# Kernel optimization log

Hardware: AMD Instinct MI355X
Metric: run time of the kernel (lower is better)

## Reference

```python
import jax, jax.numpy as jnp
import numpy as np

N_NODES = 120000  # n_entities + n_users
N_REL = 16
D = 64   # entity_dim
R = 64   # relation_dim
E = 1600000


def setup_inputs() -> dict:
    key = jax.random.key(0)
    k1, k2, k3, k4, k5, k6 = jax.random.split(key, 6)
    return {
        "entity_user_embed": jax.random.normal(k1, (N_NODES, D), dtype=jnp.float32) * 0.1,
        "relation_embed": jax.random.normal(k2, (N_REL, R), dtype=jnp.float32) * 0.1,
        "W_R": jax.random.normal(k3, (N_REL, D, R), dtype=jnp.float32) * 0.1,
        "edge_src": jax.random.randint(k4, (E,), 0, N_NODES, dtype=jnp.int32),
        "edge_dst": jax.random.randint(k5, (E,), 0, N_NODES, dtype=jnp.int32),
        "edge_type": jax.random.randint(k6, (E,), 0, N_REL, dtype=jnp.int32),
    }


def reference(entity_user_embed, relation_embed, W_R, edge_src, edge_dst, edge_type):
    n_nodes = entity_user_embed.shape[0]
    # Per-relation transform of every node embedding: [n_rel, n_nodes, R].
    # Equivalent to the per-relation edge loop: matmul(emb[id], W_R[r]).
    trans = jnp.einsum('nd,rdk->rnk', entity_user_embed, W_R)
    r_mul_t = trans[edge_type, edge_src]   # [E, R] (edges.src path)
    r_mul_h = trans[edge_type, edge_dst]   # [E, R] (edges.dst path)
    r_embed = relation_embed[edge_type]    # [E, R]
    # bmm([E,1,R], [E,R,1]) -> per-edge dot product
    att = jnp.sum(r_mul_t * jnp.tanh(r_mul_h + r_embed), axis=-1)  # [E]
    # edge softmax over incoming edges of each destination node
    att_max = jax.ops.segment_max(att, edge_dst, num_segments=n_nodes)
    ex = jnp.exp(att - att_max[edge_dst])
    denom = jax.ops.segment_sum(ex, edge_dst, num_segments=n_nodes)
    out = ex / denom[edge_dst]
    return out[:, None]  # [E, 1], matching squeeze(-1) of [E,1,1]
```

## Files before the change

kernel.cpp:

```cpp
#include <hip/hip_runtime.h>
#include <hip/hip_bf16.h>

#define D64 64
#define NREL 16
#define SCALE 32.0f
#define INV_SCALE 0.03125f

typedef __attribute__((ext_vector_type(8))) short bf16x8;
typedef __attribute__((ext_vector_type(4))) float f32x4;
typedef __attribute__((ext_vector_type(2))) float f32x2;

__device__ __forceinline__ float tanh_fast(float x) {
    float e = __expf(2.0f * x);
    return 1.0f - 2.0f / (e + 1.0f);
}

__device__ __forceinline__ float tanh_poly(float x) {
    x = fmaxf(-1.5f, fminf(1.5f, x));
    float u = x * x;
    float p = fmaf(u, -0.0182227f, 0.108952f);
    p = fmaf(u, p, -0.329139f);
    p = fmaf(u, p, 1.0f);
    return x * p;
}

__device__ __forceinline__ unsigned short f2b(float x) {
    __hip_bfloat16 h = __float2bfloat16(x);
    return *reinterpret_cast<unsigned short*>(&h);
}

__global__ void prep_kernel(const float* __restrict__ WR, const float* __restrict__ rel,
                            unsigned short* __restrict__ Wt, float* __restrict__ relp,
                            float* __restrict__ denom, int n_nodes) {
    int i = blockIdx.x * blockDim.x + threadIdx.x;
    if (i < NREL * D64 * D64) {
        int r = i >> 12, mt = (i >> 10) & 3, q2 = (i >> 9) & 1;
        int ln = (i >> 3) & 63, j = i & 7;
        int c = mt * 16 + (ln & 15);
        int d = q2 * 32 + ((ln >> 4) << 3) + j;
        Wt[i] = f2b(WR[(r << 12) + (d << 6) + c] * SCALE);
    }
    if (i < NREL * D64) {
        int t = i >> 6, kp = i & 63;
        int q = kp >> 4, m = (kp >> 2) & 3, g = kp & 3;
        relp[i] = rel[t * D64 + m * 16 + q * 4 + g];
    }
    if (i < n_nodes) denom[i] = 0.0f;
}

__global__ __launch_bounds__(256, 3)
void trans_gemm_kernel(const float* __restrict__ emb,
                       const unsigned short* __restrict__ Wt,
                       uint4* __restrict__ trans,
                       int n_nodes) {
    const int tid  = threadIdx.x;
    const int lane = tid & 63;
    const int wid  = tid >> 6;
    const int col  = lane & 15;
    const int quad = lane >> 4;
    const int rbase = (blockIdx.x & 1) * 8;
    const int nodebase = (blockIdx.x >> 1) * 256 + wid * 64;

    bf16x8 bfr[4][2];
    int nds[4];
    #pragma unroll
    for (int j = 0; j < 4; ++j) {
        int node = nodebase + j * 16 + col;
        nds[j] = node;
        int cn = node < n_nodes ? node : n_nodes - 1;
        const float* bp = emb + (size_t)cn * D64 + quad * 8;
        #pragma unroll
        for (int ks = 0; ks < 2; ++ks) {
            float4 v0 = *(const float4*)(bp + ks * 32);
            float4 v1 = *(const float4*)(bp + ks * 32 + 4);
            bfr[j][ks][0] = (short)f2b(v0.x); bfr[j][ks][1] = (short)f2b(v0.y);
            bfr[j][ks][2] = (short)f2b(v0.z); bfr[j][ks][3] = (short)f2b(v0.w);
            bfr[j][ks][4] = (short)f2b(v1.x); bfr[j][ks][5] = (short)f2b(v1.y);
            bfr[j][ks][6] = (short)f2b(v1.z); bfr[j][ks][7] = (short)f2b(v1.w);
        }
    }

    const unsigned short* wb = Wt + (rbase << 12) + (lane << 3);

    #pragma unroll 1
    for (int rr = 0; rr < 8; ++rr) {
        const int r = rbase + rr;
        const unsigned short* lb = wb + (rr << 12);
        f32x4 acc[4][4];
        #pragma unroll
        for (int mt = 0; mt < 4; ++mt) {
            bf16x8 a0 = *(const bf16x8*)(lb + (mt << 10));
            bf16x8 a1 = *(const bf16x8*)(lb + (mt << 10) + 512);
            #pragma unroll
            for (int j = 0; j < 4; ++j) {
                f32x4 c = {0.f, 0.f, 0.f, 0.f};
                c = __builtin_amdgcn_mfma_f32_16x16x32_bf16(a0, bfr[j][0], c, 0, 0, 0);
                c = __builtin_amdgcn_mfma_f32_16x16x32_bf16(a1, bfr[j][1], c, 0, 0, 0);
                acc[mt][j] = c;
            }
        }
        #pragma unroll
        for (int j = 0; j < 4; ++j) {
            if (nds[j] < n_nodes) {
                uint4 pk;
                unsigned p;
                p = __builtin_amdgcn_cvt_pk_fp8_f32(acc[0][j][0], acc[0][j][1], 0, false);
                p = __builtin_amdgcn_cvt_pk_fp8_f32(acc[0][j][2], acc[0][j][3], p, true);
                pk.x = p;
                p = __builtin_amdgcn_cvt_pk_fp8_f32(acc[1][j][0], acc[1][j][1], 0, false);
                p = __builtin_amdgcn_cvt_pk_fp8_f32(acc[1][j][2], acc[1][j][3], p, true);
                pk.y = p;
                p = __builtin_amdgcn_cvt_pk_fp8_f32(acc[2][j][0], acc[2][j][1], 0, false);
                p = __builtin_amdgcn_cvt_pk_fp8_f32(acc[2][j][2], acc[2][j][3], p, true);
                pk.z = p;
                p = __builtin_amdgcn_cvt_pk_fp8_f32(acc[3][j][0], acc[3][j][1], 0, false);
                p = __builtin_amdgcn_cvt_pk_fp8_f32(acc[3][j][2], acc[3][j][3], p, true);
                pk.w = p;
                trans[((size_t)r * n_nodes + nds[j]) * 4 + quad] = pk;
            }
        }
    }
}

__device__ __forceinline__ void term4(unsigned ut, unsigned uh, float4 r, float& acc) {
    f32x2 tlo = __builtin_amdgcn_cvt_pk_f32_fp8(ut, false);
    f32x2 thi = __builtin_amdgcn_cvt_pk_f32_fp8(ut, true);
    f32x2 hlo = __builtin_amdgcn_cvt_pk_f32_fp8(uh, false);
    f32x2 hhi = __builtin_amdgcn_cvt_pk_f32_fp8(uh, true);
    acc += tlo[0] * tanh_poly(fmaf(hlo[0], INV_SCALE, r.x));
    acc += tlo[1] * tanh_poly(fmaf(hlo[1], INV_SCALE, r.y));
    acc += thi[0] * tanh_poly(fmaf(hhi[0], INV_SCALE, r.z));
    acc += thi[1] * tanh_poly(fmaf(hhi[1], INV_SCALE, r.w));
}

__global__ __launch_bounds__(256)
void edge_kernel(const unsigned* __restrict__ trans,
                 const float* __restrict__ relp,
                 const int* __restrict__ esrc, const int* __restrict__ edst,
                 const int* __restrict__ etype,
                 float* __restrict__ out, float* __restrict__ denom,
                 int E, int n_nodes) {
    int e0 = blockIdx.x * 512 + threadIdx.x;
    int e1 = e0 + 256;
    bool v0 = e0 < E, v1 = e1 < E;
    int i0 = v0 ? e0 : 0;
    int i1 = v1 ? e1 : 0;
    int t0 = etype[i0], s0 = esrc[i0], d0 = edst[i0];
    int t1 = etype[i1], s1 = esrc[i1], d1 = edst[i1];

    const uint4* tb = (const uint4*)trans;
    unsigned nn = (unsigned)n_nodes;
    unsigned rt0 = ((unsigned)t0 * nn + (unsigned)s0) * 4u;
    unsigned rh0 = ((unsigned)t0 * nn + (unsigned)d0) * 4u;
    unsigned rt1 = ((unsigned)t1 * nn + (unsigned)s1) * 4u;
    unsigned rh1 = ((unsigned)t1 * nn + (unsigned)d1) * 4u;

    uint4 T0[4], H0[4], T1[4], H1[4];
    #pragma unroll
    for (int c4 = 0; c4 < 4; ++c4) {
        T0[c4] = tb[rt0 + c4]; H0[c4] = tb[rh0 + c4];
        T1[c4] = tb[rt1 + c4]; H1[c4] = tb[rh1 + c4];
    }

    const float4* pr0 = (const float4*)(relp + t0 * D64);
    const float4* pr1 = (const float4*)(relp + t1 * D64);
    float a0 = 0.f, a1 = 0.f;
    #pragma unroll
    for (int c4 = 0; c4 < 4; ++c4) {
        term4(T0[c4].x, H0[c4].x, pr0[c4 * 4 + 0], a0);
        term4(T1[c4].x, H1[c4].x, pr1[c4 * 4 + 0], a1);
        term4(T0[c4].y, H0[c4].y, pr0[c4 * 4 + 1], a0);
        term4(T1[c4].y, H1[c4].y, pr1[c4 * 4 + 1], a1);
        term4(T0[c4].z, H0[c4].z, pr0[c4 * 4 + 2], a0);
        term4(T1[c4].z, H1[c4].z, pr1[c4 * 4 + 2], a1);
        term4(T0[c4].w, H0[c4].w, pr0[c4 * 4 + 3], a0);
        term4(T1[c4].w, H1[c4].w, pr1[c4 * 4 + 3], a1);
    }
    if (v0) {
        float ex = __expf(a0 * INV_SCALE);
        out[e0] = ex;
        atomicAdd(&denom[d0], ex);
    }
    if (v1) {
        float ex = __expf(a1 * INV_SCALE);
        out[e1] = ex;
        atomicAdd(&denom[d1], ex);
    }
}

__global__ void normalize_kernel(float* __restrict__ out,
                                 const float* __restrict__ denom,
                                 const int* __restrict__ edst, int E) {
    int e = blockIdx.x * blockDim.x + threadIdx.x;
    if (e < E) out[e] = out[e] / denom[edst[e]];
}

__global__ void zero_denom_kernel(float* __restrict__ denom, int n) {
    int i = blockIdx.x * blockDim.x + threadIdx.x;
    if (i < n) denom[i] = 0.0f;
}

__global__ __launch_bounds__(256)
void edge_att_fallback(const float* __restrict__ emb, const float* __restrict__ rel,
                       const float* __restrict__ WR, const int* __restrict__ esrc,
                       const int* __restrict__ edst, const int* __restrict__ etype,
                       float* __restrict__ exbuf, float* __restrict__ denom,
                       int E, int chunkSize) {
    const int type = blockIdx.x & 15;
    const int c    = blockIdx.x >> 4;
    const int lane = threadIdx.x & 63;
    const int wid  = threadIdx.x >> 6;
    long base0 = (long)c * (long)chunkSize;
    long cend  = base0 + chunkSize;
    if (cend > E) cend = E;
    if (base0 >= cend) return;
    int per = (chunkSize + 3) >> 2;
    long wbeg = base0 + (long)wid * per;
    long wend = wbeg + per;
    if (wend > cend) wend = cend;
    if (wbeg >= wend) return;
    float w[D64];
    const float* Wt = WR + (size_t)type * D64 * D64;
    #pragma unroll
    for (int d = 0; d < D64; ++d) w[d] = Wt[d * D64 + lane];
    const float rk = rel[type * D64 + lane];
    for (long s0 = wbeg; s0 < wend; s0 += 64) {
        long e = s0 + lane;
        int ty = -1, sv = 0, dv = 0;
        if (e < wend) { ty = etype[e]; sv = esrc[e]; dv = edst[e]; }
        unsigned long long m = __ballot(ty == type);
        while (m) {
            int b = __builtin_ctzll(m);
            m &= m - 1;
            int sn = __builtin_amdgcn_readlane(sv, b);
            int dn = __builtin_amdgcn_readlane(dv, b);
            const float4* es4 = (const float4*)(emb + (size_t)sn * D64);
            const float4* ed4 = (const float4*)(emb + (size_t)dn * D64);
            float t0 = 0.f, t1 = 0.f, t2 = 0.f, t3 = 0.f;
            float h0 = 0.f, h1 = 0.f, h2 = 0.f, h3 = 0.f;
            #pragma unroll
            for (int i = 0; i < D64 / 4; ++i) {
                float4 a = es4[i]; float4 b4 = ed4[i];
                t0 = fmaf(a.x, w[4*i+0], t0); t1 = fmaf(a.y, w[4*i+1], t1);
                t2 = fmaf(a.z, w[4*i+2], t2); t3 = fmaf(a.w, w[4*i+3], t3);
                h0 = fmaf(b4.x, w[4*i+0], h0); h1 = fmaf(b4.y, w[4*i+1], h1);
                h2 = fmaf(b4.z, w[4*i+2], h2); h3 = fmaf(b4.w, w[4*i+3], h3);
            }
            float t = (t0 + t1) + (t2 + t3);
            float h = (h0 + h1) + (h2 + h3);
            float p = t * tanh_fast(h + rk);
            #pragma unroll
            for (int off = 32; off > 0; off >>= 1) p += __shfl_xor(p, off);
            if (lane == 0) {
                float ex = __expf(p);
                exbuf[s0 + b] = ex;
                atomicAdd(&denom[dn], ex);
            }
        }
    }
}

__global__ void normalize_fallback(float* __restrict__ out,
                                   const float* __restrict__ denom,
                                   const int* __restrict__ edst, int E) {
    int e = blockIdx.x * blockDim.x + threadIdx.x;
    if (e < E) out[e] = out[e] / denom[edst[e]];
}

extern "C" void kernel_launch(void* const* d_in, const int* in_sizes, int n_in,
                              void* d_out, int out_size, void* d_ws, size_t ws_size,
                              hipStream_t stream) {
    const float* emb  = (const float*)d_in[0];
    const float* rel  = (const float*)d_in[1];
    const float* WR   = (const float*)d_in[2];
    const int*   esrc = (const int*)d_in[3];
    const int*   edst = (const int*)d_in[4];
    const int*   ety  = (const int*)d_in[5];

    const int E       = in_sizes[3];
    const int n_nodes = in_sizes[0] / D64;
    float* out = (float*)d_out;

    size_t transB = (size_t)NREL * n_nodes * D64;
    size_t off_trans = 0;
    size_t off_wt    = (off_trans + transB + 255) & ~(size_t)255;
    size_t off_rel   = (off_wt + (size_t)NREL * D64 * D64 * 2 + 255) & ~(size_t)255;
    size_t off_den   = (off_rel + (size_t)NREL * D64 * 4 + 255) & ~(size_t)255;
    size_t need      = off_den + (size_t)n_nodes * sizeof(float);

    if (ws_size >= need) {
        uint4*          trans = (uint4*)((char*)d_ws + off_trans);
        unsigned short* Wt    = (unsigned short*)((char*)d_ws + off_wt);
        float*          relp  = (float*)((char*)d_ws + off_rel);
        float*          denom = (float*)((char*)d_ws + off_den);

        int prepN = n_nodes > NREL * D64 * D64 ? n_nodes : NREL * D64 * D64;
        prep_kernel<<<(prepN + 255) / 256, 256, 0, stream>>>(WR, rel, Wt, relp,
                                                             denom, n_nodes);
        trans_gemm_kernel<<<((n_nodes + 255) / 256) * 2, 256, 0, stream>>>(emb, Wt, trans, n_nodes);
        edge_kernel<<<(E + 511) / 512, 256, 0, stream>>>((const unsigned*)trans, relp,
                                                         esrc, edst, ety,
                                                         out, denom, E, n_nodes);
        normalize_kernel<<<(E + 255) / 256, 256, 0, stream>>>(out, denom, edst, E);
    } else {
        float* denom = (float*)d_ws;
        zero_denom_kernel<<<(n_nodes + 255) / 256, 256, 0, stream>>>(denom, n_nodes);
        const int NCHUNK = 256;
        int chunk = (E + NCHUNK - 1) / NCHUNK;
        edge_att_fallback<<<16 * NCHUNK, 256, 0, stream>>>(emb, rel, WR, esrc, edst, ety,
                                                           out, denom, E, chunk);
        normalize_fallback<<<(E + 255) / 256, 256, 0, stream>>>(out, denom, edst, E);
    }
}
```

Measured before the change: 238.0 us.

## Bucket edges by relation type before the attention gather kernel

Adds a three-kernel counting sort (histogram, scan, scatter) that groups edges by relation type. The edge kernel then reads src/dst/type from the sorted arrays and writes results back through the original edge index. Its blocks are also remapped with an XCD-aware swizzle so each region of the per-relation trans table is gathered by fewer L2 domains. The goal is better cache locality for the random trans gathers, paid for with extra index traffic, a scattered output write, and several new launches including a single-block scan.

```diff
diff --git a/kernel.cpp b/kernel.cpp
--- a/kernel.cpp
+++ b/kernel.cpp
@@ -5,6 +5,7 @@
 #define NREL 16
 #define SCALE 32.0f
 #define INV_SCALE 0.03125f
+#define PNB 256
 
 typedef __attribute__((ext_vector_type(8))) short bf16x8;
 typedef __attribute__((ext_vector_type(4))) float f32x4;
@@ -131,6 +132,131 @@
     acc += tlo[1] * tanh_poly(fmaf(hlo[1], INV_SCALE, r.y));
     acc += thi[0] * tanh_poly(fmaf(hhi[0], INV_SCALE, r.z));
     acc += thi[1] * tanh_poly(fmaf(hhi[1], INV_SCALE, r.w));
+}
+
+
+__global__ __launch_bounds__(256)
+void hist_kernel(const int* __restrict__ etype, int* __restrict__ cnt,
+                 int E, int chunk) {
+    __shared__ int h[NREL];
+    int tid = threadIdx.x;
+    if (tid < NREL) h[tid] = 0;
+    __syncthreads();
+    int beg = blockIdx.x * chunk;
+    int end = beg + chunk; if (end > E) end = E;
+    for (int e = beg + tid; e < end; e += 256)
+        atomicAdd(&h[etype[e]], 1);
+    __syncthreads();
+    if (tid < NREL) cnt[blockIdx.x * NREL + tid] = h[tid];
+}
+
+__global__ __launch_bounds__(256)
+void scan_kernel(const int* __restrict__ cnt, int* __restrict__ base) {
+    __shared__ int lc[PNB * NREL];
+    __shared__ int tt[NREL], tb[NREL];
+    int tid = threadIdx.x;
+    for (int i = tid; i < PNB * NREL; i += 256) lc[i] = cnt[i];
+    __syncthreads();
+    if (tid < NREL) {
+        int s = 0;
+        for (int b = 0; b < PNB; ++b) s += lc[b * NREL + tid];
+        tt[tid] = s;
+    }
+    __syncthreads();
+    if (tid == 0) {
+        int run = 0;
+        for (int t = 0; t < NREL; ++t) { tb[t] = run; run += tt[t]; }
+    }
+    __syncthreads();
+    if (tid < NREL) {
+        int run = tb[tid];
+        for (int b = 0; b < PNB; ++b) {
+            int c = lc[b * NREL + tid];
+            lc[b * NREL + tid] = run;
+            run += c;
+        }
+    }
+    __syncthreads();
+    for (int i = tid; i < PNB * NREL; i += 256) base[i] = lc[i];
+}
+
+__global__ __launch_bounds__(256)
+void scatter_kernel(const int* __restrict__ esrc, const int* __restrict__ edst,
+                    const int* __restrict__ etype, const int* __restrict__ base,
+                    int* __restrict__ bsrc, int* __restrict__ bdst,
+                    int* __restrict__ btype, int* __restrict__ borig,
+                    int E, int chunk) {
+    __shared__ int cur[NREL];
+    int tid = threadIdx.x;
+    if (tid < NREL) cur[tid] = base[blockIdx.x * NREL + tid];
+    __syncthreads();
+    int beg = blockIdx.x * chunk;
+    int end = beg + chunk; if (end > E) end = E;
+    for (int e = beg + tid; e < end; e += 256) {
+        int t = etype[e];
+        int pos = atomicAdd(&cur[t], 1);
+        bsrc[pos]  = esrc[e];
+        bdst[pos]  = edst[e];
+        btype[pos] = t;
+        borig[pos] = e;
+    }
+}
+
+__global__ __launch_bounds__(256)
+void edge_bucketed_kernel(const unsigned* __restrict__ trans,
+                          const float* __restrict__ relp,
+                          const int* __restrict__ bsrc, const int* __restrict__ bdst,
+                          const int* __restrict__ btype, const int* __restrict__ borig,
+                          float* __restrict__ out, float* __restrict__ denom,
+                          int E, int n_nodes) {
+    int q = gridDim.x >> 3;
+    int wg = ((int)blockIdx.x & 7) * q + ((int)blockIdx.x >> 3);
+    int e0 = wg * 512 + threadIdx.x;
+    int e1 = e0 + 256;
+    bool v0 = e0 < E, v1 = e1 < E;
+    int i0 = v0 ? e0 : 0;
+    int i1 = v1 ? e1 : 0;
+    int t0 = btype[i0], s0 = bsrc[i0], d0 = bdst[i0], o0 = borig[i0];
+    int t1 = btype[i1], s1 = bsrc[i1], d1 = bdst[i1], o1 = borig[i1];
+
+    const uint4* tb = (const uint4*)trans;
+    unsigned nn = (unsigned)n_nodes;
+    unsigned rt0 = ((unsigned)t0 * nn + (unsigned)s0) * 4u;
+    unsigned rh0 = ((unsigned)t0 * nn + (unsigned)d0) * 4u;
+    unsigned rt1 = ((unsigned)t1 * nn + (unsigned)s1) * 4u;
+    unsigned rh1 = ((unsigned)t1 * nn + (unsigned)d1) * 4u;
+
+    uint4 T0[4], H0[4], T1[4], H1[4];
+    #pragma unroll
+    for (int c4 = 0; c4 < 4; ++c4) {
+        T0[c4] = tb[rt0 + c4]; H0[c4] = tb[rh0 + c4];
+        T1[c4] = tb[rt1 + c4]; H1[c4] = tb[rh1 + c4];
+    }
+
+    const float4* pr0 = (const float4*)(relp + t0 * D64);
+    const float4* pr1 = (const float4*)(relp + t1 * D64);
+    float a0 = 0.f, a1 = 0.f;
+    #pragma unroll
+    for (int c4 = 0; c4 < 4; ++c4) {
+        term4(T0[c4].x, H0[c4].x, pr0[c4 * 4 + 0], a0);
+        term4(T1[c4].x, H1[c4].x, pr1[c4 * 4 + 0], a1);
+        term4(T0[c4].y, H0[c4].y, pr0[c4 * 4 + 1], a0);
+        term4(T1[c4].y, H1[c4].y, pr1[c4 * 4 + 1], a1);
+        term4(T0[c4].z, H0[c4].z, pr0[c4 * 4 + 2], a0);
+        term4(T1[c4].z, H1[c4].z, pr1[c4 * 4 + 2], a1);
+        term4(T0[c4].w, H0[c4].w, pr0[c4 * 4 + 3], a0);
+        term4(T1[c4].w, H1[c4].w, pr1[c4 * 4 + 3], a1);
+    }
+    if (v0) {
+        float ex = __expf(a0 * INV_SCALE);
+        out[o0] = ex;
+        atomicAdd(&denom[d0], ex);
+    }
+    if (v1) {
+        float ex = __expf(a1 * INV_SCALE);
+        out[o1] = ex;
+        atomicAdd(&denom[d1], ex);
+    }
 }
 
 __global__ __launch_bounds__(256)
@@ -286,9 +412,16 @@
     size_t off_wt    = (off_trans + transB + 255) & ~(size_t)255;
     size_t off_rel   = (off_wt + (size_t)NREL * D64 * D64 * 2 + 255) & ~(size_t)255;
     size_t off_den   = (off_rel + (size_t)NREL * D64 * 4 + 255) & ~(size_t)255;
-    size_t need      = off_den + (size_t)n_nodes * sizeof(float);
-
-    if (ws_size >= need) {
+    size_t need_basic = off_den + (size_t)n_nodes * sizeof(float);
+    size_t off_bsrc  = (need_basic + 255) & ~(size_t)255;
+    size_t off_bdst  = (off_bsrc + (size_t)E * 4 + 255) & ~(size_t)255;
+    size_t off_btyp  = (off_bdst + (size_t)E * 4 + 255) & ~(size_t)255;
+    size_t off_borg  = (off_btyp + (size_t)E * 4 + 255) & ~(size_t)255;
+    size_t off_cnt   = (off_borg + (size_t)E * 4 + 255) & ~(size_t)255;
+    size_t off_base  = (off_cnt + (size_t)PNB * NREL * 4 + 255) & ~(size_t)255;
+    size_t need_bucket = off_base + (size_t)PNB * NREL * 4;
+
+    if (ws_size >= need_basic) {
         uint4*          trans = (uint4*)((char*)d_ws + off_trans);
         unsigned short* Wt    = (unsigned short*)((char*)d_ws + off_wt);
         float*          relp  = (float*)((char*)d_ws + off_rel);
@@ -298,9 +431,29 @@
         prep_kernel<<<(prepN + 255) / 256, 256, 0, stream>>>(WR, rel, Wt, relp,
                                                              denom, n_nodes);
         trans_gemm_kernel<<<((n_nodes + 255) / 256) * 2, 256, 0, stream>>>(emb, Wt, trans, n_nodes);
-        edge_kernel<<<(E + 511) / 512, 256, 0, stream>>>((const unsigned*)trans, relp,
-                                                         esrc, edst, ety,
-                                                         out, denom, E, n_nodes);
+
+        if (ws_size >= need_bucket) {
+            int* bsrc  = (int*)((char*)d_ws + off_bsrc);
+            int* bdst  = (int*)((char*)d_ws + off_bdst);
+            int* btyp  = (int*)((char*)d_ws + off_btyp);
+            int* borg  = (int*)((char*)d_ws + off_borg);
+            int* cnt   = (int*)((char*)d_ws + off_cnt);
+            int* base  = (int*)((char*)d_ws + off_base);
+            int chunk  = (E + PNB - 1) / PNB;
+            hist_kernel<<<PNB, 256, 0, stream>>>(ety, cnt, E, chunk);
+            scan_kernel<<<1, 256, 0, stream>>>(cnt, base);
+            scatter_kernel<<<PNB, 256, 0, stream>>>(esrc, edst, ety, base,
+                                                    bsrc, bdst, btyp, borg, E, chunk);
+            int gb = (E + 511) / 512;
+            int gpad = ((gb + 7) / 8) * 8;
+            edge_bucketed_kernel<<<gpad, 256, 0, stream>>>((const unsigned*)trans, relp,
+                                                           bsrc, bdst, btyp, borg,
+                                                           out, denom, E, n_nodes);
+        } else {
+            edge_kernel<<<(E + 511) / 512, 256, 0, stream>>>((const unsigned*)trans, relp,
+                                                             esrc, edst, ety,
+                                                             out, denom, E, n_nodes);
+        }
         normalize_kernel<<<(E + 255) / 256, 256, 0, stream>>>(out, denom, edst, E);
     } else {
         float* denom = (float*)d_ws;
```

Result: slower. 268.9 us (+13.0%).

## Gather each edge's fp8 rows cooperatively across four lanes with shuffle reduction

Applied to the files above, without the earlier changes.

The edge kernel now has groups of four lanes share the row offsets of eight edges through shuffles. Each lane loads one 16-byte quarter of each 64-byte fp8 row, and the partial dot products are combined with xor shuffles. The aim is to turn scattered per-thread 64-byte gathers into contiguous 64-byte segments per lane group, improving memory coalescing. In exchange it adds shuffle traffic, reductions, and a per-edge relation-vector load.

```diff
diff --git a/kernel.cpp b/kernel.cpp
--- a/kernel.cpp
+++ b/kernel.cpp
@@ -9,6 +9,7 @@
 typedef __attribute__((ext_vector_type(8))) short bf16x8;
 typedef __attribute__((ext_vector_type(4))) float f32x4;
 typedef __attribute__((ext_vector_type(2))) float f32x2;
+typedef __attribute__((ext_vector_type(4))) unsigned int u32x4;
 
 __device__ __forceinline__ float tanh_fast(float x) {
     float e = __expf(2.0f * x);
@@ -134,55 +135,76 @@
 }
 
 __global__ __launch_bounds__(256)
-void edge_kernel(const unsigned* __restrict__ trans,
-                 const float* __restrict__ relp,
-                 const int* __restrict__ esrc, const int* __restrict__ edst,
-                 const int* __restrict__ etype,
-                 float* __restrict__ out, float* __restrict__ denom,
-                 int E, int n_nodes) {
-    int e0 = blockIdx.x * 512 + threadIdx.x;
-    int e1 = e0 + 256;
+void edge_coop_kernel(const unsigned* __restrict__ trans,
+                      const float* __restrict__ relp,
+                      const int* __restrict__ esrc, const int* __restrict__ edst,
+                      const int* __restrict__ etype,
+                      float* __restrict__ out, float* __restrict__ denom,
+                      int E, int n_nodes) {
+    const int tid  = threadIdx.x;
+    const int lane = tid & 63;
+    const int wid  = tid >> 6;
+    const int wb   = blockIdx.x * 512 + wid * 128;
+    const int c    = lane & 3;
+
+    int e0 = wb + ((lane >> 2) << 3) + (c << 1);
+    int e1 = e0 + 1;
     bool v0 = e0 < E, v1 = e1 < E;
     int i0 = v0 ? e0 : 0;
     int i1 = v1 ? e1 : 0;
     int t0 = etype[i0], s0 = esrc[i0], d0 = edst[i0];
     int t1 = etype[i1], s1 = esrc[i1], d1 = edst[i1];
 
-    const uint4* tb = (const uint4*)trans;
     unsigned nn = (unsigned)n_nodes;
-    unsigned rt0 = ((unsigned)t0 * nn + (unsigned)s0) * 4u;
-    unsigned rh0 = ((unsigned)t0 * nn + (unsigned)d0) * 4u;
-    unsigned rt1 = ((unsigned)t1 * nn + (unsigned)s1) * 4u;
-    unsigned rh1 = ((unsigned)t1 * nn + (unsigned)d1) * 4u;
-
-    uint4 T0[4], H0[4], T1[4], H1[4];
-    #pragma unroll
-    for (int c4 = 0; c4 < 4; ++c4) {
-        T0[c4] = tb[rt0 + c4]; H0[c4] = tb[rh0 + c4];
-        T1[c4] = tb[rt1 + c4]; H1[c4] = tb[rh1 + c4];
-    }
-
-    const float4* pr0 = (const float4*)(relp + t0 * D64);
-    const float4* pr1 = (const float4*)(relp + t1 * D64);
-    float a0 = 0.f, a1 = 0.f;
-    #pragma unroll
-    for (int c4 = 0; c4 < 4; ++c4) {
-        term4(T0[c4].x, H0[c4].x, pr0[c4 * 4 + 0], a0);
-        term4(T1[c4].x, H1[c4].x, pr1[c4 * 4 + 0], a1);
-        term4(T0[c4].y, H0[c4].y, pr0[c4 * 4 + 1], a0);
-        term4(T1[c4].y, H1[c4].y, pr1[c4 * 4 + 1], a1);
-        term4(T0[c4].z, H0[c4].z, pr0[c4 * 4 + 2], a0);
-        term4(T1[c4].z, H1[c4].z, pr1[c4 * 4 + 2], a1);
-        term4(T0[c4].w, H0[c4].w, pr0[c4 * 4 + 3], a0);
-        term4(T1[c4].w, H1[c4].w, pr1[c4 * 4 + 3], a1);
-    }
+    unsigned rT0 = ((unsigned)t0 * nn + (unsigned)s0) * 64u;
+    unsigned rH0 = ((unsigned)t0 * nn + (unsigned)d0) * 64u;
+    unsigned rT1 = ((unsigned)t1 * nn + (unsigned)s1) * 64u;
+    unsigned rH1 = ((unsigned)t1 * nn + (unsigned)d1) * 64u;
+
+    const char* tbase = (const char*)trans;
+    const int grp0 = lane & ~3;
+    const unsigned cb = (unsigned)(c << 4);
+
+    unsigned offT[8], offH[8];
+    int tt[8];
+    #pragma unroll
+    for (int k = 0; k < 8; ++k) {
+        int sl = grp0 + (k >> 1);
+        offT[k] = (unsigned)__shfl((int)((k & 1) ? rT1 : rT0), sl, 64) + cb;
+        offH[k] = (unsigned)__shfl((int)((k & 1) ? rH1 : rH0), sl, 64) + cb;
+        tt[k]   = __shfl((k & 1) ? t1 : t0, sl, 64);
+    }
+
+    u32x4 T[8], H[8];
+    #pragma unroll
+    for (int k = 0; k < 8; ++k) {
+        T[k] = *(const u32x4*)(tbase + offT[k]);
+        H[k] = *(const u32x4*)(tbase + offH[k]);
+    }
+
+    float sum0 = 0.f, sum1 = 0.f;
+    #pragma unroll
+    for (int k = 0; k < 8; ++k) {
+        const float4* pr = (const float4*)(relp + tt[k] * D64 + (c << 4));
+        float a = 0.f;
+        term4(T[k][0], H[k][0], pr[0], a);
+        term4(T[k][1], H[k][1], pr[1], a);
+        term4(T[k][2], H[k][2], pr[2], a);
+        term4(T[k][3], H[k][3], pr[3], a);
+        a += __shfl_xor(a, 1, 64);
+        a += __shfl_xor(a, 2, 64);
+        if (c == (k >> 1)) {
+            if (k & 1) sum1 = a; else sum0 = a;
+        }
+    }
+
     if (v0) {
-        float ex = __expf(a0 * INV_SCALE);
+        float ex = __expf(sum0 * INV_SCALE);
         out[e0] = ex;
         atomicAdd(&denom[d0], ex);
     }
     if (v1) {
-        float ex = __expf(a1 * INV_SCALE);
+        float ex = __expf(sum1 * INV_SCALE);
         out[e1] = ex;
         atomicAdd(&denom[d1], ex);
     }
@@ -298,9 +320,9 @@
         prep_kernel<<<(prepN + 255) / 256, 256, 0, stream>>>(WR, rel, Wt, relp,
                                                              denom, n_nodes);
         trans_gemm_kernel<<<((n_nodes + 255) / 256) * 2, 256, 0, stream>>>(emb, Wt, trans, n_nodes);
-        edge_kernel<<<(E + 511) / 512, 256, 0, stream>>>((const unsigned*)trans, relp,
-                                                         esrc, edst, ety,
-                                                         out, denom, E, n_nodes);
+        edge_coop_kernel<<<(E + 511) / 512, 256, 0, stream>>>((const unsigned*)trans, relp,
+                                                              esrc, edst, ety,
+                                                              out, denom, E, n_nodes);
         normalize_kernel<<<(E + 255) / 256, 256, 0, stream>>>(out, denom, edst, E);
     } else {
         float* denom = (float*)d_ws;
```

New measurement: 225.3 us. 1.06x faster.
